# Kernel tuning notes

Measured on AMD Instinct MI355X. Metric: run time of the kernel, lower is better.

## Reference

```python
import jax, jax.numpy as jnp
import numpy as np

N = 100_000   # nodes
E = 1_600_000 # edges per relation (avg degree 16)
IN, H, O = 128, 128, 128


def _graph_conv(x, src, dst, W, b, relu):
    """DGL GraphConv, norm='both': y = D_dst^{-1/2} A D_src^{-1/2} x W + b."""
    ones = jnp.ones(src.shape[0], dtype=x.dtype)
    deg_out = jnp.clip(jax.ops.segment_sum(ones, src, num_segments=N), 1.0)  # [N]
    deg_in = jnp.clip(jax.ops.segment_sum(ones, dst, num_segments=N), 1.0)   # [N]
    h = (x * (deg_out ** -0.5)[:, None]) @ W                 # [N, out] transform first (in==out)
    agg = jax.ops.segment_sum(h[src], dst, num_segments=N)   # SpMM: gather + scatter-add
    y = agg * (deg_in ** -0.5)[:, None] + b
    return jax.nn.relu(y) if relu else y


def setup_inputs() -> dict:
    key = jax.random.key(0)
    ks = jax.random.split(key, 8)
    g = 0.1  # weight scale ~ xavier for d=128
    return {
        "x": jax.random.normal(ks[0], (N, IN), dtype=jnp.float32),
        "src_i": jax.random.randint(ks[1], (E,), 0, N),
        "dst_i": jax.random.randint(ks[2], (E,), 0, N),
        "src_b": jax.random.randint(ks[3], (E,), 0, N),
        "dst_b": jax.random.randint(ks[4], (E,), 0, N),
        "W1_i": jax.random.normal(ks[5], (IN, H), dtype=jnp.float32) * g,
        "b1_i": jnp.zeros((H,), dtype=jnp.float32),
        "W1_b": jax.random.normal(ks[6], (IN, H), dtype=jnp.float32) * g,
        "b1_b": jnp.zeros((H,), dtype=jnp.float32),
        "W2": jax.random.normal(ks[7], (H, O), dtype=jnp.float32) * g,
        "b2": jnp.zeros((O,), dtype=jnp.float32),
    }


def reference(x, src_i, dst_i, src_b, dst_b, W1_i, b1_i, W1_b, b1_b, W2, b2):
    # conv1: HeteroGraphConv({'interacts','behave'}, aggregate='sum'), ReLU inside each conv
    h = (_graph_conv(x, src_i, dst_i, W1_i, b1_i, relu=True)
         + _graph_conv(x, src_b, dst_b, W1_b, b1_b, relu=True))
    # conv2: only 'interacts', no activation
    return _graph_conv(h, src_i, dst_i, W2, b2, relu=False)
```

## Files before the change

kernel.cpp:

```cpp
#include <hip/hip_runtime.h>
#include <hip/hip_fp16.h>

#define N_NODES 100000
#define N_EDGES 1600000
#define XB 64
#define CHUNK (N_EDGES / XB)
#define HSH 2
#define HBINS (N_NODES / HSH)
#define PSH 128
#define PBINS ((N_NODES + PSH - 1) / PSH)
#define PCAP 16384
#define TILE 4096
#define WT_LD 136

typedef _Float16 half8_t __attribute__((ext_vector_type(8)));
typedef float f32x4 __attribute__((ext_vector_type(4)));
typedef unsigned long long u64;

__device__ inline unsigned packh2(float a, float b) {
  __half2 h = __floats2half2_rn(a, b);
  return *(unsigned*)&h;
}

__global__ __launch_bounds__(256) void k_hist(
    const int* __restrict__ src_i, const int* __restrict__ src_b,
    unsigned* __restrict__ part32) {
  __shared__ unsigned h[HBINS / 4];
  const int xb = blockIdx.x, job = blockIdx.y, sl = blockIdx.z;
  const int* arr = job ? src_b : src_i;
  const int lo = sl * HBINS;
  for (int i = threadIdx.x; i < HBINS / 4; i += 256) h[i] = 0;
  __syncthreads();
  const int4* a4 = (const int4*)(arr + xb * CHUNK);
  for (int q = threadIdx.x; q < CHUNK / 4; q += 256) {
    int4 v = a4[q];
    int t;
    t = v.x - lo; if ((unsigned)t < HBINS) atomicAdd(&h[t >> 2], 1u << ((t & 3) * 8));
    t = v.y - lo; if ((unsigned)t < HBINS) atomicAdd(&h[t >> 2], 1u << ((t & 3) * 8));
    t = v.z - lo; if ((unsigned)t < HBINS) atomicAdd(&h[t >> 2], 1u << ((t & 3) * 8));
    t = v.w - lo; if ((unsigned)t < HBINS) atomicAdd(&h[t >> 2], 1u << ((t & 3) * 8));
  }
  __syncthreads();
  unsigned* dst = part32 + ((size_t)(job * XB + xb) * N_NODES + lo) / 4;
  for (int i = threadIdx.x; i < HBINS / 4; i += 256) dst[i] = h[i];
}

__global__ __launch_bounds__(256) void k_hred(
    const unsigned* __restrict__ part32,
    float* __restrict__ dso_i, float* __restrict__ dso_b) {
  const int b4 = blockIdx.x * 256 + threadIdx.x;
  if (b4 >= N_NODES / 4) return;
  const int b0 = b4 * 4;
  const size_t Q = N_NODES / 4;
  int s0, s1, s2, s3;
  s0 = s1 = s2 = s3 = 0;
  for (int xb = 0; xb < XB; ++xb) {
    unsigned w = part32[(size_t)(0 * XB + xb) * Q + b4];
    s0 += w & 255; s1 += (w >> 8) & 255; s2 += (w >> 16) & 255; s3 += w >> 24;
  }
  dso_i[b0] = rsqrtf((float)max(s0, 1)); dso_i[b0 + 1] = rsqrtf((float)max(s1, 1));
  dso_i[b0 + 2] = rsqrtf((float)max(s2, 1)); dso_i[b0 + 3] = rsqrtf((float)max(s3, 1));
  s0 = s1 = s2 = s3 = 0;
  for (int xb = 0; xb < XB; ++xb) {
    unsigned w = part32[(size_t)(1 * XB + xb) * Q + b4];
    s0 += w & 255; s1 += (w >> 8) & 255; s2 += (w >> 16) & 255; s3 += w >> 24;
  }
  dso_b[b0] = rsqrtf((float)max(s0, 1)); dso_b[b0 + 1] = rsqrtf((float)max(s1, 1));
  dso_b[b0 + 2] = rsqrtf((float)max(s2, 1)); dso_b[b0 + 3] = rsqrtf((float)max(s3, 1));
}

__global__ __launch_bounds__(256) void k_bucket(
    const int* __restrict__ src_i, const int* __restrict__ dst_i,
    const int* __restrict__ src_b, const int* __restrict__ dst_b,
    int* __restrict__ bcur, u64* __restrict__ pairs) {
  __shared__ u64 stage[TILE];
  __shared__ int cnt[PSH], excl[PSH], gbase[PSH], lpos[PSH], sa[PSH], sb[PSH];
  const int rel = blockIdx.y;
  const int* src = rel ? src_b : src_i;
  const int* dst = rel ? dst_b : dst_i;
  const int tid = threadIdx.x;
  const int base = blockIdx.x * TILE;
  const int nE = min(TILE, N_EDGES - base);

  for (int i = tid; i < PSH; i += 256) { cnt[i] = 0; lpos[i] = 0; }
  __syncthreads();

  u64 ed[16];
  int eb[16];
#pragma unroll
  for (int j = 0; j < 16; ++j) {
    int idx = base + j * 256 + tid;
    if (idx < N_EDGES && (j * 256 + tid) < nE) {
      int s = src[idx], d = dst[idx];
      ed[j] = ((u64)(unsigned)d << 32) | (unsigned)s;
      eb[j] = d / PBINS;
      atomicAdd(&cnt[eb[j]], 1);
    } else {
      eb[j] = -1;
    }
  }
  __syncthreads();
  if (tid < PSH) sa[tid] = cnt[tid];
  __syncthreads();
  int* p = sa;
  int* q = sb;
  for (int d = 1; d < PSH; d <<= 1) {
    if (tid < PSH) q[tid] = ((tid >= d) ? p[tid - d] : 0) + p[tid];
    __syncthreads();
    int* tmp = p; p = q; q = tmp;
  }
  if (tid < PSH) {
    excl[tid] = p[tid] - cnt[tid];
    gbase[tid] = atomicAdd(&bcur[rel * PSH + tid], cnt[tid]);
  }
  __syncthreads();
#pragma unroll
  for (int j = 0; j < 16; ++j) {
    if (eb[j] >= 0) {
      int pos = excl[eb[j]] + atomicAdd(&lpos[eb[j]], 1);
      stage[pos] = ed[j];
    }
  }
  __syncthreads();
  for (int i = tid; i < nE; i += 256) {
    u64 e = stage[i];
    int b = (int)(e >> 32) / PBINS;
    pairs[(size_t)(rel * PSH + b) * PCAP + gbase[b] + (i - excl[b])] = e;
  }
}

__global__ void k_bprefix(const int* __restrict__ bcur, int* __restrict__ bbase,
                          int* __restrict__ off_i, int* __restrict__ off_b) {
  __shared__ int ws[2][2];
  const int tid = threadIdx.x;
  const int rel = tid >> 7, i = tid & 127;
  const int lane = tid & 63;
  const int w2 = (tid >> 6) & 1;
  int v = bcur[rel * PSH + i];
  int x = v;
#pragma unroll
  for (int d = 1; d < 64; d <<= 1) {
    int t = __shfl_up(x, d);
    if (lane >= d) x += t;
  }
  if (lane == 63) ws[rel][w2] = x;
  __syncthreads();
  int addv = (w2 == 1) ? ws[rel][0] : 0;
  bbase[rel * PSH + i] = x - v + addv;
  if (tid == 0) { off_i[N_NODES] = N_EDGES; off_b[N_NODES] = N_EDGES; }
}

__global__ __launch_bounds__(256) void k_fill2(
    const int* __restrict__ bcur, const int* __restrict__ bbase,
    const u64* __restrict__ pairs,
    int* __restrict__ off_i, int* __restrict__ off_b,
    float* __restrict__ dsi_i, float* __restrict__ dsi_b,
    int* __restrict__ es_i, int* __restrict__ es_b) {
  __shared__ int cnt[PBINS];
  __shared__ int wsum[4];
  const int b = blockIdx.x, rel = blockIdx.y;
  const int lo = b * PBINS;
  const int hi = min(lo + PBINS, N_NODES);
  const int bins = hi - lo;
  int* off = rel ? off_b : off_i;
  float* dsi = rel ? dsi_b : dsi_i;
  int* es = rel ? es_b : es_i;
  const u64* seg = pairs + (size_t)(rel * PSH + b) * PCAP;
  const int nb = bcur[rel * PSH + b];
  const int base = bbase[rel * PSH + b];
  const int tid = threadIdx.x;
  for (int i = tid; i < bins; i += 256) cnt[i] = 0;
  __syncthreads();
  for (int i = tid; i < nb; i += 256) {
    int d = (int)(seg[i] >> 32);
    atomicAdd(&cnt[d - lo], 1);
  }
  __syncthreads();
  const int i0 = tid * 4;
  int v[4];
#pragma unroll
  for (int k = 0; k < 4; ++k) v[k] = (i0 + k < bins) ? cnt[i0 + k] : 0;
  int tl = v[0] + v[1] + v[2] + v[3];
  const int lane = tid & 63, wid = tid >> 6;
  int x = tl;
#pragma unroll
  for (int d = 1; d < 64; d <<= 1) {
    int t = __shfl_up(x, d);
    if (lane >= d) x += t;
  }
  if (lane == 63) wsum[wid] = x;
  __syncthreads();
  int wb = 0;
#pragma unroll
  for (int w = 0; w < 4; ++w)
    if (w < wid) wb += wsum[w];
  int run = wb + x - tl;
#pragma unroll
  for (int k = 0; k < 4; ++k) {
    if (i0 + k < bins) {
      off[lo + i0 + k] = base + run;
      dsi[lo + i0 + k] = rsqrtf((float)max(v[k], 1));
      cnt[i0 + k] = run;
    }
    run += v[k];
  }
  __syncthreads();
  for (int i = tid; i < nb; i += 256) {
    u64 e = seg[i];
    int d = (int)(e >> 32);
    int p = atomicAdd(&cnt[d - lo], 1);
    es[base + p] = (int)(unsigned)e;
  }
}

__global__ __launch_bounds__(256) void k_gemm_mfma(
    const float* __restrict__ A,
    const float* __restrict__ Wa, const float* __restrict__ Wb,
    const float* __restrict__ rsa, const float* __restrict__ rsb,
    unsigned short* __restrict__ Ca, unsigned short* __restrict__ Cb) {
  __shared__ unsigned short shw[128 * WT_LD];
  const int rel = blockIdx.y;
  const float* W = rel ? Wb : Wa;
  const float* rs = rel ? rsb : rsa;
  unsigned short* C = rel ? Cb : Ca;

  for (int t = threadIdx.x; t < 2048; t += 256) {
    int c4 = (t & 31) * 4;
    int k = (t >> 5) * 2;
    float4 w0 = *(const float4*)&W[k * 128 + c4];
    float4 w1 = *(const float4*)&W[(k + 1) * 128 + c4];
    *(unsigned*)&shw[(c4 + 0) * WT_LD + k] = packh2(w0.x, w1.x);
    *(unsigned*)&shw[(c4 + 1) * WT_LD + k] = packh2(w0.y, w1.y);
    *(unsigned*)&shw[(c4 + 2) * WT_LD + k] = packh2(w0.z, w1.z);
    *(unsigned*)&shw[(c4 + 3) * WT_LD + k] = packh2(w0.w, w1.w);
  }
  __syncthreads();

  const int w = threadIdx.x >> 6;
  const int l = threadIdx.x & 63;
  const int lc = l & 15;
  const int lk = l >> 4;
  const int rb = blockIdx.x * 128 + w * 32;

  f32x4 acc[2][8];
#pragma unroll
  for (int rf = 0; rf < 2; ++rf)
#pragma unroll
    for (int cf = 0; cf < 8; ++cf) acc[rf][cf] = (f32x4)(0.f);

  union H8 { unsigned u[4]; half8_t h; };

#pragma unroll
  for (int kc = 0; kc < 4; ++kc) {
    const int kbase = kc * 32 + lk * 8;
    H8 a[2];
#pragma unroll
    for (int rf = 0; rf < 2; ++rf) {
      int row = rb + rf * 16 + lc;
      row = min(row, N_NODES - 1);
      const float4* ap = (const float4*)(A + (size_t)row * 128 + kbase);
      float4 f0 = ap[0], f1 = ap[1];
      a[rf].u[0] = packh2(f0.x, f0.y);
      a[rf].u[1] = packh2(f0.z, f0.w);
      a[rf].u[2] = packh2(f1.x, f1.y);
      a[rf].u[3] = packh2(f1.z, f1.w);
    }
#pragma unroll
    for (int cf = 0; cf < 8; ++cf) {
      half8_t b = *(const half8_t*)&shw[(cf * 16 + lc) * WT_LD + kbase];
      acc[0][cf] = __builtin_amdgcn_mfma_f32_16x16x32_f16(a[0].h, b, acc[0][cf], 0, 0, 0);
      acc[1][cf] = __builtin_amdgcn_mfma_f32_16x16x32_f16(a[1].h, b, acc[1][cf], 0, 0, 0);
    }
  }

#pragma unroll
  for (int rf = 0; rf < 2; ++rf) {
#pragma unroll
    for (int reg = 0; reg < 4; ++reg) {
      int row = rb + rf * 16 + lk * 4 + reg;
      if (row < N_NODES) {
        float s = rs[row];
        unsigned short* crow = C + (size_t)row * 128 + lc;
#pragma unroll
        for (int cf = 0; cf < 8; ++cf) {
          __half h = __float2half_rn(acc[rf][cf][reg] * s);
          crow[cf * 16] = *(unsigned short*)&h;
        }
      }
    }
  }
}

__device__ inline void spmm_acc(const uint4* __restrict__ Xv, const int* __restrict__ srcs,
                                int e0, int e1, int l, float* a) {
  int e = e0;
  for (; e + 16 <= e1; e += 16) {
    int s = srcs[e + l];
    uint4 v[16];
#pragma unroll
    for (int j = 0; j < 16; ++j) v[j] = Xv[(size_t)__shfl(s, j, 16) * 16 + l];
#pragma unroll
    for (int j = 0; j < 16; ++j) {
      float2 f;
      f = __half22float2(*(__half2*)&v[j].x); a[0] += f.x; a[1] += f.y;
      f = __half22float2(*(__half2*)&v[j].y); a[2] += f.x; a[3] += f.y;
      f = __half22float2(*(__half2*)&v[j].z); a[4] += f.x; a[5] += f.y;
      f = __half22float2(*(__half2*)&v[j].w); a[6] += f.x; a[7] += f.y;
    }
  }
  if (e < e1) {
    int s = (e + l < e1) ? srcs[e + l] : 0;
    int cnt = e1 - e;
    for (int j = 0; j < cnt; ++j) {
      uint4 v = Xv[(size_t)__shfl(s, j, 16) * 16 + l];
      float2 f;
      f = __half22float2(*(__half2*)&v.x); a[0] += f.x; a[1] += f.y;
      f = __half22float2(*(__half2*)&v.y); a[2] += f.x; a[3] += f.y;
      f = __half22float2(*(__half2*)&v.z); a[4] += f.x; a[5] += f.y;
      f = __half22float2(*(__half2*)&v.w); a[6] += f.x; a[7] += f.y;
    }
  }
}

__global__ __launch_bounds__(256) void k_spmm_l1(
    const unsigned short* __restrict__ Xi, const int* __restrict__ off_i,
    const int* __restrict__ es_i, const float* __restrict__ dsi_i,
    const float* __restrict__ b_i,
    const unsigned short* __restrict__ Xb, const int* __restrict__ off_b,
    const int* __restrict__ es_b, const float* __restrict__ dsi_b,
    const float* __restrict__ b_b, float* __restrict__ out) {
  const int g = threadIdx.x >> 4;
  const int l = threadIdx.x & 15;
  const int n = blockIdx.x * 16 + g;
  if (n >= N_NODES) return;
  float y[8];
  {
    float a[8] = {0.f, 0.f, 0.f, 0.f, 0.f, 0.f, 0.f, 0.f};
    spmm_acc((const uint4*)Xi, es_i, off_i[n], off_i[n + 1], l, a);
    const float dn = dsi_i[n];
    float4 c0 = ((const float4*)b_i)[l * 2];
    float4 c1 = ((const float4*)b_i)[l * 2 + 1];
    y[0] = fmaxf(fmaf(a[0], dn, c0.x), 0.f); y[1] = fmaxf(fmaf(a[1], dn, c0.y), 0.f);
    y[2] = fmaxf(fmaf(a[2], dn, c0.z), 0.f); y[3] = fmaxf(fmaf(a[3], dn, c0.w), 0.f);
    y[4] = fmaxf(fmaf(a[4], dn, c1.x), 0.f); y[5] = fmaxf(fmaf(a[5], dn, c1.y), 0.f);
    y[6] = fmaxf(fmaf(a[6], dn, c1.z), 0.f); y[7] = fmaxf(fmaf(a[7], dn, c1.w), 0.f);
  }
  {
    float a[8] = {0.f, 0.f, 0.f, 0.f, 0.f, 0.f, 0.f, 0.f};
    spmm_acc((const uint4*)Xb, es_b, off_b[n], off_b[n + 1], l, a);
    const float dn = dsi_b[n];
    float4 c0 = ((const float4*)b_b)[l * 2];
    float4 c1 = ((const float4*)b_b)[l * 2 + 1];
    y[0] += fmaxf(fmaf(a[0], dn, c0.x), 0.f); y[1] += fmaxf(fmaf(a[1], dn, c0.y), 0.f);
    y[2] += fmaxf(fmaf(a[2], dn, c0.z), 0.f); y[3] += fmaxf(fmaf(a[3], dn, c0.w), 0.f);
    y[4] += fmaxf(fmaf(a[4], dn, c1.x), 0.f); y[5] += fmaxf(fmaf(a[5], dn, c1.y), 0.f);
    y[6] += fmaxf(fmaf(a[6], dn, c1.z), 0.f); y[7] += fmaxf(fmaf(a[7], dn, c1.w), 0.f);
  }
  float4* ov = (float4*)out;
  size_t oi = (size_t)n * 32 + l * 2;
  ov[oi] = make_float4(y[0], y[1], y[2], y[3]);
  ov[oi + 1] = make_float4(y[4], y[5], y[6], y[7]);
}

__global__ __launch_bounds__(256) void k_spmm_l2(
    const unsigned short* __restrict__ Xh, const int* __restrict__ off,
    const int* __restrict__ srcs, const float* __restrict__ dsi,
    const float* __restrict__ bias, float* __restrict__ out) {
  const int g = threadIdx.x >> 4;
  const int l = threadIdx.x & 15;
  const int n = blockIdx.x * 16 + g;
  if (n >= N_NODES) return;
  float a[8] = {0.f, 0.f, 0.f, 0.f, 0.f, 0.f, 0.f, 0.f};
  spmm_acc((const uint4*)Xh, srcs, off[n], off[n + 1], l, a);
  const float dn = dsi[n];
  float4 c0 = ((const float4*)bias)[l * 2];
  float4 c1 = ((const float4*)bias)[l * 2 + 1];
  float4 y0, y1;
  y0.x = fmaf(a[0], dn, c0.x); y0.y = fmaf(a[1], dn, c0.y);
  y0.z = fmaf(a[2], dn, c0.z); y0.w = fmaf(a[3], dn, c0.w);
  y1.x = fmaf(a[4], dn, c1.x); y1.y = fmaf(a[5], dn, c1.y);
  y1.z = fmaf(a[6], dn, c1.z); y1.w = fmaf(a[7], dn, c1.w);
  float4* ov = (float4*)out;
  size_t oi = (size_t)n * 32 + l * 2;
  ov[oi] = y0;
  ov[oi + 1] = y1;
}

extern "C" void kernel_launch(void* const* d_in, const int* in_sizes, int n_in,
                              void* d_out, int out_size, void* d_ws, size_t ws_size,
                              hipStream_t stream) {
  const float* x    = (const float*)d_in[0];
  const int* src_i  = (const int*)d_in[1];
  const int* dst_i  = (const int*)d_in[2];
  const int* src_b  = (const int*)d_in[3];
  const int* dst_b  = (const int*)d_in[4];
  const float* W1_i = (const float*)d_in[5];
  const float* b1_i = (const float*)d_in[6];
  const float* W1_b = (const float*)d_in[7];
  const float* b1_b = (const float*)d_in[8];
  const float* W2   = (const float*)d_in[9];
  const float* b2   = (const float*)d_in[10];
  float* out = (float*)d_out;

  char* ws = (char*)d_ws;
  size_t o = 0;
  auto alloc = [&](size_t bytes) {
    char* p = ws + o;
    o += (bytes + 255) & ~(size_t)255;
    return p;
  };
  float* dso_i = (float*)alloc(N_NODES * 4);
  float* dsi_i = (float*)alloc(N_NODES * 4);
  float* dso_b = (float*)alloc(N_NODES * 4);
  float* dsi_b = (float*)alloc(N_NODES * 4);
  int* off_i = (int*)alloc((N_NODES + 1) * 4);
  int* off_b = (int*)alloc((N_NODES + 1) * 4);
  int* bcur = (int*)alloc(2 * PSH * 4);
  int* bbase = (int*)alloc(2 * PSH * 4);
  int* es_i = (int*)alloc((size_t)N_EDGES * 4);
  int* es_b = (int*)alloc((size_t)N_EDGES * 4);
  char* uni = alloc((size_t)2 * N_NODES * 128 * 2);
  unsigned* part32      = (unsigned*)uni;
  u64* pairs            = (u64*)uni;
  unsigned short* buf_i = (unsigned short*)uni;
  unsigned short* buf_b = (unsigned short*)(uni + (size_t)N_NODES * 128 * 2);
  (void)ws_size; (void)in_sizes; (void)n_in; (void)out_size;

  hipMemsetAsync(bcur, 0, 2 * PSH * 4, stream);
  k_hist<<<dim3(XB, 2, HSH), dim3(256), 0, stream>>>(src_i, src_b, part32);
  k_hred<<<(N_NODES / 4 + 255) / 256, dim3(256), 0, stream>>>(part32, dso_i, dso_b);
  k_bucket<<<dim3((N_EDGES + TILE - 1) / TILE, 2), dim3(256), 0, stream>>>(
      src_i, dst_i, src_b, dst_b, bcur, pairs);
  k_bprefix<<<1, 256, 0, stream>>>(bcur, bbase, off_i, off_b);
  k_fill2<<<dim3(PSH, 2), dim3(256), 0, stream>>>(
      bcur, bbase, pairs, off_i, off_b, dsi_i, dsi_b, es_i, es_b);

  const int ggrid = (N_NODES + 127) / 128;
  const int sgrid = (N_NODES + 15) / 16;
  k_gemm_mfma<<<dim3(ggrid, 2), dim3(256), 0, stream>>>(
      x, W1_i, W1_b, dso_i, dso_b, buf_i, buf_b);
  k_spmm_l1<<<sgrid, 256, 0, stream>>>(
      buf_i, off_i, es_i, dsi_i, b1_i, buf_b, off_b, es_b, dsi_b, b1_b, out);
  k_gemm_mfma<<<dim3(ggrid, 1), dim3(256), 0, stream>>>(
      out, W2, W2, dso_i, dso_i, buf_i, buf_i);
  k_spmm_l2<<<sgrid, 256, 0, stream>>>(buf_i, off_i, es_i, dsi_i, b2, out);
}
```

Measured before the change: 459.6 us.

## Store layer-1 hidden as fp16 and pack bucket pairs into 32-bit words

The layer-1 SpMM now writes its hidden activations as fp16 into the output buffer instead of fp32. A new GEMM variant reads those fp16 rows directly into MFMA, which halves the write and read traffic for the intermediate. Bucket pairs are also packed into 32-bit words, holding the local destination offset in the high bits and a 17-bit source, replacing 64-bit pairs. That halves scratch traffic in the CSR build. The cost is fp16 rounding of the intermediate and the assumption that node ids fit in 17 bits.

```diff
diff --git a/kernel.cpp b/kernel.cpp
--- a/kernel.cpp
+++ b/kernel.cpp
@@ -72,7 +72,7 @@
 __global__ __launch_bounds__(256) void k_bucket(
     const int* __restrict__ src_i, const int* __restrict__ dst_i,
     const int* __restrict__ src_b, const int* __restrict__ dst_b,
-    int* __restrict__ bcur, u64* __restrict__ pairs) {
+    int* __restrict__ bcur, unsigned* __restrict__ pairs) {
   __shared__ u64 stage[TILE];
   __shared__ int cnt[PSH], excl[PSH], gbase[PSH], lpos[PSH], sa[PSH], sb[PSH];
   const int rel = blockIdx.y;
@@ -124,8 +124,10 @@
   __syncthreads();
   for (int i = tid; i < nE; i += 256) {
     u64 e = stage[i];
-    int b = (int)(e >> 32) / PBINS;
-    pairs[(size_t)(rel * PSH + b) * PCAP + gbase[b] + (i - excl[b])] = e;
+    int d = (int)(e >> 32);
+    int b = d / PBINS;
+    unsigned pk = ((unsigned)(d - b * PBINS) << 17) | (unsigned)(e & 0x1FFFFu);
+    pairs[(size_t)(rel * PSH + b) * PCAP + gbase[b] + (i - excl[b])] = pk;
   }
 }
 
@@ -152,7 +154,7 @@
 
 __global__ __launch_bounds__(256) void k_fill2(
     const int* __restrict__ bcur, const int* __restrict__ bbase,
-    const u64* __restrict__ pairs,
+    const unsigned* __restrict__ pairs,
     int* __restrict__ off_i, int* __restrict__ off_b,
     float* __restrict__ dsi_i, float* __restrict__ dsi_b,
     int* __restrict__ es_i, int* __restrict__ es_b) {
@@ -165,15 +167,15 @@
   int* off = rel ? off_b : off_i;
   float* dsi = rel ? dsi_b : dsi_i;
   int* es = rel ? es_b : es_i;
-  const u64* seg = pairs + (size_t)(rel * PSH + b) * PCAP;
+  const unsigned* seg = pairs + (size_t)(rel * PSH + b) * PCAP;
   const int nb = bcur[rel * PSH + b];
   const int base = bbase[rel * PSH + b];
   const int tid = threadIdx.x;
   for (int i = tid; i < bins; i += 256) cnt[i] = 0;
   __syncthreads();
   for (int i = tid; i < nb; i += 256) {
-    int d = (int)(seg[i] >> 32);
-    atomicAdd(&cnt[d - lo], 1);
+    int dl = (int)(seg[i] >> 17);
+    atomicAdd(&cnt[dl], 1);
   }
   __syncthreads();
   const int i0 = tid * 4;
@@ -206,10 +208,10 @@
   }
   __syncthreads();
   for (int i = tid; i < nb; i += 256) {
-    u64 e = seg[i];
-    int d = (int)(e >> 32);
-    int p = atomicAdd(&cnt[d - lo], 1);
-    es[base + p] = (int)(unsigned)e;
+    unsigned e = seg[i];
+    int dl = (int)(e >> 17);
+    int p = atomicAdd(&cnt[dl], 1);
+    es[base + p] = (int)(e & 0x1FFFFu);
   }
 }
 
@@ -291,6 +293,71 @@
   }
 }
 
+__global__ __launch_bounds__(256) void k_gemm_mfma_h(
+    const unsigned short* __restrict__ Ah,
+    const float* __restrict__ W, const float* __restrict__ rs,
+    unsigned short* __restrict__ C) {
+  __shared__ unsigned short shw[128 * WT_LD];
+  for (int t = threadIdx.x; t < 2048; t += 256) {
+    int c4 = (t & 31) * 4;
+    int k = (t >> 5) * 2;
+    float4 w0 = *(const float4*)&W[k * 128 + c4];
+    float4 w1 = *(const float4*)&W[(k + 1) * 128 + c4];
+    *(unsigned*)&shw[(c4 + 0) * WT_LD + k] = packh2(w0.x, w1.x);
+    *(unsigned*)&shw[(c4 + 1) * WT_LD + k] = packh2(w0.y, w1.y);
+    *(unsigned*)&shw[(c4 + 2) * WT_LD + k] = packh2(w0.z, w1.z);
+    *(unsigned*)&shw[(c4 + 3) * WT_LD + k] = packh2(w0.w, w1.w);
+  }
+  __syncthreads();
+
+  const int w = threadIdx.x >> 6;
+  const int l = threadIdx.x & 63;
+  const int lc = l & 15;
+  const int lk = l >> 4;
+  const int rb = blockIdx.x * 128 + w * 32;
+
+  f32x4 acc[2][8];
+#pragma unroll
+  for (int rf = 0; rf < 2; ++rf)
+#pragma unroll
+    for (int cf = 0; cf < 8; ++cf) acc[rf][cf] = (f32x4)(0.f);
+
+#pragma unroll
+  for (int kc = 0; kc < 4; ++kc) {
+    const int kbase = kc * 32 + lk * 8;
+    half8_t a[2];
+#pragma unroll
+    for (int rf = 0; rf < 2; ++rf) {
+      int row = rb + rf * 16 + lc;
+      row = min(row, N_NODES - 1);
+      a[rf] = *(const half8_t*)&Ah[(size_t)row * 128 + kbase];
+    }
+#pragma unroll
+    for (int cf = 0; cf < 8; ++cf) {
+      half8_t b = *(const half8_t*)&shw[(cf * 16 + lc) * WT_LD + kbase];
+      acc[0][cf] = __builtin_amdgcn_mfma_f32_16x16x32_f16(a[0], b, acc[0][cf], 0, 0, 0);
+      acc[1][cf] = __builtin_amdgcn_mfma_f32_16x16x32_f16(a[1], b, acc[1][cf], 0, 0, 0);
+    }
+  }
+
+#pragma unroll
+  for (int rf = 0; rf < 2; ++rf) {
+#pragma unroll
+    for (int reg = 0; reg < 4; ++reg) {
+      int row = rb + rf * 16 + lk * 4 + reg;
+      if (row < N_NODES) {
+        float s = rs[row];
+        unsigned short* crow = C + (size_t)row * 128 + lc;
+#pragma unroll
+        for (int cf = 0; cf < 8; ++cf) {
+          __half h = __float2half_rn(acc[rf][cf][reg] * s);
+          crow[cf * 16] = *(unsigned short*)&h;
+        }
+      }
+    }
+  }
+}
+
 __device__ inline void spmm_acc(const uint4* __restrict__ Xv, const int* __restrict__ srcs,
                                 int e0, int e1, int l, float* a) {
   int e = e0;
@@ -328,7 +395,7 @@
     const float* __restrict__ b_i,
     const unsigned short* __restrict__ Xb, const int* __restrict__ off_b,
     const int* __restrict__ es_b, const float* __restrict__ dsi_b,
-    const float* __restrict__ b_b, float* __restrict__ out) {
+    const float* __restrict__ b_b, unsigned short* __restrict__ hout) {
   const int g = threadIdx.x >> 4;
   const int l = threadIdx.x & 15;
   const int n = blockIdx.x * 16 + g;
@@ -356,10 +423,12 @@
     y[4] += fmaxf(fmaf(a[4], dn, c1.x), 0.f); y[5] += fmaxf(fmaf(a[5], dn, c1.y), 0.f);
     y[6] += fmaxf(fmaf(a[6], dn, c1.z), 0.f); y[7] += fmaxf(fmaf(a[7], dn, c1.w), 0.f);
   }
-  float4* ov = (float4*)out;
-  size_t oi = (size_t)n * 32 + l * 2;
-  ov[oi] = make_float4(y[0], y[1], y[2], y[3]);
-  ov[oi + 1] = make_float4(y[4], y[5], y[6], y[7]);
+  uint4 hw;
+  hw.x = packh2(y[0], y[1]);
+  hw.y = packh2(y[2], y[3]);
+  hw.z = packh2(y[4], y[5]);
+  hw.w = packh2(y[6], y[7]);
+  ((uint4*)hout)[(size_t)n * 16 + l] = hw;
 }
 
 __global__ __launch_bounds__(256) void k_spmm_l2(
@@ -401,6 +470,7 @@
   const float* W2   = (const float*)d_in[9];
   const float* b2   = (const float*)d_in[10];
   float* out = (float*)d_out;
+  unsigned short* hbuf = (unsigned short*)d_out;
 
   char* ws = (char*)d_ws;
   size_t o = 0;
@@ -421,7 +491,7 @@
   int* es_b = (int*)alloc((size_t)N_EDGES * 4);
   char* uni = alloc((size_t)2 * N_NODES * 128 * 2);
   unsigned* part32      = (unsigned*)uni;
-  u64* pairs            = (u64*)uni;
+  unsigned* pairs       = (unsigned*)uni;
   unsigned short* buf_i = (unsigned short*)uni;
   unsigned short* buf_b = (unsigned short*)(uni + (size_t)N_NODES * 128 * 2);
   (void)ws_size; (void)in_sizes; (void)n_in; (void)out_size;
@@ -440,8 +510,7 @@
   k_gemm_mfma<<<dim3(ggrid, 2), dim3(256), 0, stream>>>(
       x, W1_i, W1_b, dso_i, dso_b, buf_i, buf_b);
   k_spmm_l1<<<sgrid, 256, 0, stream>>>(
-      buf_i, off_i, es_i, dsi_i, b1_i, buf_b, off_b, es_b, dsi_b, b1_b, out);
-  k_gemm_mfma<<<dim3(ggrid, 1), dim3(256), 0, stream>>>(
-      out, W2, W2, dso_i, dso_i, buf_i, buf_i);
+      buf_i, off_i, es_i, dsi_i, b1_i, buf_b, off_b, es_b, dsi_b, b1_b, hbuf);
+  k_gemm_mfma_h<<<dim3(ggrid), dim3(256), 0, stream>>>(hbuf, W2, dso_i, buf_i);
   k_spmm_l2<<<sgrid, 256, 0, stream>>>(buf_i, off_i, es_i, dsi_i, b2, out);
 }
```

Measured after the change: 456.1 us. No clear change (-0.8%).
